# Performance work log

Hardware: AMD Instinct MI355X
Metric: run time of the kernel (lower is better)

## Reference

```python
import jax, jax.numpy as jnp
import numpy as np

B, T, C = 1024, 50, 66   # batch, frames, motion dim
H = 1024                 # LSTM state size
EPS = 1e-5               # LN_v2 epsilon


def _lstm_cell(x, h, c, W_ih, W_hh, b):
    # PyTorch gate order: input, forget, cell, output
    g = x @ W_ih.T + h @ W_hh.T + b            # [B, 4H]
    i, f, gg, o = jnp.split(g, 4, axis=-1)
    i = jax.nn.sigmoid(i)
    f = jax.nn.sigmoid(f)
    gg = jnp.tanh(gg)
    o = jax.nn.sigmoid(o)
    c2 = f * c + i * gg
    h2 = o * jnp.tanh(c2)
    return h2, c2


def setup_inputs() -> dict:
    key = jax.random.key(0)
    ks = jax.random.split(key, 12)
    s = 1.0 / np.sqrt(H)  # PyTorch LSTM init range
    return {
        "x": jax.random.normal(ks[0], (B, T, C), jnp.float32),
        # layer 0 (input_size=C); b folds PyTorch b_ih + b_hh (same math)
        "W_ih0": jax.random.uniform(ks[1], (4 * H, C), jnp.float32, -s, s),
        "W_hh0": jax.random.uniform(ks[2], (4 * H, H), jnp.float32, -s, s),
        "b0": jax.random.uniform(ks[3], (4 * H,), jnp.float32, -s, s),
        # layer 1 (input_size=H)
        "W_ih1": jax.random.uniform(ks[4], (4 * H, H), jnp.float32, -s, s),
        "W_hh1": jax.random.uniform(ks[5], (4 * H, H), jnp.float32, -s, s),
        "b1": jax.random.uniform(ks[6], (4 * H,), jnp.float32, -s, s),
        # fc0: xavier with gain 1e-8 -> near-zero weights; small scale here
        "fc_w": jax.random.normal(ks[7], (C, H), jnp.float32) * 1e-3,
        "fc_b": jnp.zeros((C,), jnp.float32),
        # LN_v2 params
        "alpha": jnp.ones((C,), jnp.float32),
        "beta": jnp.zeros((C,), jnp.float32),
    }


def reference(x, W_ih0, W_hh0, b0, W_ih1, W_hh1, b1, fc_w, fc_b, alpha, beta):
    z = jnp.zeros((x.shape[0], H), x.dtype)

    def stack(xt, h0, c0, h1, c1):
        h0, c0 = _lstm_cell(xt, h0, c0, W_ih0, W_hh0, b0)
        h1, c1 = _lstm_cell(h0, h1, c1, W_ih1, W_hh1, b1)
        return h0, c0, h1, c1

    # Encoder: consume x[:, :-1, :], keep final (h, c) of both layers
    def enc_step(carry, xt):
        return stack(xt, *carry), None

    carry, _ = jax.lax.scan(enc_step, (z, z, z, z),
                            jnp.swapaxes(x[:, :-1, :], 0, 1))

    def ln(v):  # LN_v2: layernorm over last dim, learnable alpha/beta
        m = v.mean(-1, keepdims=True)
        var = ((v - m) ** 2).mean(-1, keepdims=True)
        return (v - m) / jnp.sqrt(var + EPS) * alpha + beta

    def dec_step(carry, _):
        h0, c0, h1, c1, dec = carry
        h0, c0, h1, c1 = stack(dec, h0, c0, h1, c1)
        delta = h1 @ fc_w.T + fc_b            # fc0
        new = ln(delta) + dec                 # recursive_residual=True
        return (h0, c0, h1, c1, new), new

    dec0 = x[:, -1, :]
    _, outs = jax.lax.scan(dec_step, carry + (dec0,), None, length=x.shape[1])
    return jnp.swapaxes(outs, 0, 1)           # [B, T, C]
```

## Files before the change

### kernel.cpp

```cpp
#include <hip/hip_runtime.h>
#include <cstdint>
#include <cmath>

typedef unsigned short u16;
typedef __bf16 v8bf __attribute__((ext_vector_type(8)));
typedef float v4f __attribute__((ext_vector_type(4)));

__device__ __forceinline__ u16 f2bf(float f) {
    unsigned int u = __float_as_uint(f);
    u += 0x7fffu + ((u >> 16) & 1u);
    return (u16)(u >> 16);
}
__device__ __forceinline__ float sigmoidf_(float x) { return 1.0f / (1.0f + __expf(-x)); }
__device__ __forceinline__ float tanhf_(float x) {
    float e = __expf(2.0f * x);
    return 1.0f - 2.0f / (e + 1.0f);
}

__global__ __launch_bounds__(256)
void lstm_gemm(const u16* __restrict__ A1, int K1, int S1,
               const u16* __restrict__ A2, int S2,
               const u16* __restrict__ W, int Ktot,
               const float* __restrict__ bias,
               float* __restrict__ Cst,
               u16* __restrict__ Hout)
{
    __shared__ alignas(16) float smem[64 * 132];
    u16* At = (u16*)smem;
    u16* Bt = At + 64 * 64;

    const int tid  = threadIdx.x;
    const int wave = tid >> 6;
    const int lane = tid & 63;
    const int l16  = lane & 15;
    const int lq   = lane >> 4;
    const int wr   = wave >> 1;
    const int wc   = wave & 1;
    const int m0   = blockIdx.y * 64;
    const int n0   = blockIdx.x * 128;

    v4f acc[2][4];
#pragma unroll
    for (int i = 0; i < 2; ++i)
#pragma unroll
        for (int j = 0; j < 4; ++j) acc[i][j] = (v4f){0.f, 0.f, 0.f, 0.f};

    for (int k0 = 0; k0 < Ktot; k0 += 64) {
        const u16* Asrc; int kof, st;
        if (k0 < K1) { Asrc = A1; kof = k0;      st = S1; }
        else         { Asrc = A2; kof = k0 - K1; st = S2; }
#pragma unroll
        for (int r = 0; r < 2; ++r) {
            int c = tid + r * 256;
            int row = c >> 3;
            int kc  = (c & 7) ^ (row & 7);
            const u16* g = Asrc + (size_t)(m0 + row) * st + kof + kc * 8;
            __builtin_amdgcn_global_load_lds(
                (const __attribute__((address_space(1))) unsigned int*)g,
                (__attribute__((address_space(3))) unsigned int*)(At + c * 8),
                16, 0, 0);
        }
#pragma unroll
        for (int r = 0; r < 4; ++r) {
            int c = tid + r * 256;
            int row = c >> 3;
            int kc  = (c & 7) ^ (row & 7);
            const u16* g = W + (size_t)(n0 + row) * Ktot + k0 + kc * 8;
            __builtin_amdgcn_global_load_lds(
                (const __attribute__((address_space(1))) unsigned int*)g,
                (__attribute__((address_space(3))) unsigned int*)(Bt + c * 8),
                16, 0, 0);
        }
        asm volatile("s_waitcnt vmcnt(0)" ::: "memory");
        __syncthreads();

#pragma unroll
        for (int kk = 0; kk < 64; kk += 32) {
            const int kcb = kk >> 3;
            v8bf a[2], b[4];
#pragma unroll
            for (int mi = 0; mi < 2; ++mi) {
                int row = wr * 32 + mi * 16 + l16;
                int p = row * 8 + ((kcb + lq) ^ (row & 7));
                a[mi] = *(const v8bf*)(At + p * 8);
            }
#pragma unroll
            for (int ni = 0; ni < 4; ++ni) {
                int row = wc * 64 + ni * 16 + l16;
                int p = row * 8 + ((kcb + lq) ^ (row & 7));
                b[ni] = *(const v8bf*)(Bt + p * 8);
            }
#pragma unroll
            for (int mi = 0; mi < 2; ++mi)
#pragma unroll
                for (int ni = 0; ni < 4; ++ni)
                    acc[mi][ni] = __builtin_amdgcn_mfma_f32_16x16x32_bf16(
                        a[mi], b[ni], acc[mi][ni], 0, 0, 0);
        }
        __syncthreads();
    }

    float* gates = smem;
#pragma unroll
    for (int mi = 0; mi < 2; ++mi)
#pragma unroll
        for (int ni = 0; ni < 4; ++ni) {
            int col = wc * 64 + ni * 16 + l16;
            float bs = bias[n0 + col];
#pragma unroll
            for (int r = 0; r < 4; ++r) {
                int row = wr * 32 + mi * 16 + lq * 4 + r;
                gates[row * 132 + col] = acc[mi][ni][r] + bs;
            }
        }
    __syncthreads();

#pragma unroll
    for (int it = tid; it < 64 * 32; it += 256) {
        int row = it >> 5, u = it & 31;
        const float* gp = gates + row * 132 + u * 4;
        float gi = gp[0], gf = gp[1], gg = gp[2], go = gp[3];
        int b = m0 + row;
        int U = (n0 >> 2) + u;
        float c  = Cst[b * 1024 + U];
        float i_ = sigmoidf_(gi);
        float f_ = sigmoidf_(gf);
        float g_ = tanhf_(gg);
        float o_ = sigmoidf_(go);
        float c2 = f_ * c + i_ * g_;
        float h  = o_ * tanhf_(c2);
        Cst[b * 1024 + U]  = c2;
        Hout[b * 1024 + U] = f2bf(h);
    }
}

__global__ __launch_bounds__(256)
void fc_ln_kernel(const u16* __restrict__ H1, const u16* __restrict__ Wf,
                  const float* __restrict__ fcb, const float* __restrict__ alpha,
                  const float* __restrict__ beta,
                  const float* __restrict__ decprev, float* __restrict__ outp,
                  u16* __restrict__ decnext)
{
    const int tid  = threadIdx.x;
    const int wave = tid >> 6, lane = tid & 63;
    const int l16  = lane & 15, lq = lane >> 4;
    const int b0   = blockIdx.x * 64 + wave * 16;

    v4f acc[5];
#pragma unroll
    for (int i = 0; i < 5; ++i) acc[i] = (v4f){0.f, 0.f, 0.f, 0.f};

    for (int k = 0; k < 1024; k += 32) {
        v8bf a = *(const v8bf*)(H1 + (size_t)(b0 + l16) * 1024 + k + lq * 8);
#pragma unroll
        for (int ni = 0; ni < 5; ++ni) {
            v8bf bb = *(const v8bf*)(Wf + (size_t)(ni * 16 + l16) * 1024 + k + lq * 8);
            acc[ni] = __builtin_amdgcn_mfma_f32_16x16x32_bf16(a, bb, acc[ni], 0, 0, 0);
        }
    }

    float av[5], bv[5], fb[5]; int valid[5];
#pragma unroll
    for (int ni = 0; ni < 5; ++ni) {
        int col = ni * 16 + l16;
        valid[ni] = col < 66;
        fb[ni] = valid[ni] ? fcb[col]   : 0.f;
        av[ni] = valid[ni] ? alpha[col] : 0.f;
        bv[ni] = valid[ni] ? beta[col]  : 0.f;
    }
#pragma unroll
    for (int r = 0; r < 4; ++r) {
        int b = b0 + lq * 4 + r;
        float d[5];
        float s = 0.f;
#pragma unroll
        for (int ni = 0; ni < 5; ++ni) {
            d[ni] = valid[ni] ? (acc[ni][r] + fb[ni]) : 0.f;
            s += d[ni];
        }
#pragma unroll
        for (int m = 1; m < 16; m <<= 1) s += __shfl_xor(s, m, 64);
        float mean = s * (1.f / 66.f);
        float vs = 0.f;
#pragma unroll
        for (int ni = 0; ni < 5; ++ni) {
            float t = valid[ni] ? (d[ni] - mean) : 0.f;
            vs += t * t;
        }
#pragma unroll
        for (int m = 1; m < 16; m <<= 1) vs += __shfl_xor(vs, m, 64);
        float inv = rsqrtf(vs * (1.f / 66.f) + 1e-5f);
#pragma unroll
        for (int ni = 0; ni < 5; ++ni) {
            if (valid[ni]) {
                int col = ni * 16 + l16;
                float y = (d[ni] - mean) * inv * av[ni] + bv[ni]
                        + decprev[(size_t)b * 3300 + col];
                outp[(size_t)b * 3300 + col] = y;
                decnext[b * 128 + col] = f2bf(y);
            }
        }
    }
}

__global__ void k_init_w0(const float* __restrict__ Wih, const float* __restrict__ Whh,
                          u16* __restrict__ Wc)
{
    int idx = blockIdx.x * 256 + threadIdx.x;
    if (idx >= 4096 * 1152) return;
    int jp = idx / 1152, k = idx - jp * 1152;
    int u = jp >> 2, g = jp & 3;
    float v = 0.f;
    if (k < 66)        v = Wih[(g * 1024 + u) * 66 + k];
    else if (k >= 128) v = Whh[(size_t)(g * 1024 + u) * 1024 + (k - 128)];
    Wc[idx] = f2bf(v);
}
__global__ void k_init_w1(const float* __restrict__ Wih, const float* __restrict__ Whh,
                          u16* __restrict__ Wc)
{
    int idx = blockIdx.x * 256 + threadIdx.x;
    int jp = idx >> 11, k = idx & 2047;
    int u = jp >> 2, g = jp & 3;
    float v = (k < 1024) ? Wih[(size_t)(g * 1024 + u) * 1024 + k]
                         : Whh[(size_t)(g * 1024 + u) * 1024 + (k - 1024)];
    Wc[idx] = f2bf(v);
}
__global__ void k_init_fcw(const float* __restrict__ fcw, u16* __restrict__ Wb)
{
    int idx = blockIdx.x * 256 + threadIdx.x;
    int r = idx >> 10, k = idx & 1023;
    float v = (r < 66) ? fcw[(size_t)r * 1024 + k] : 0.f;
    Wb[idx] = f2bf(v);
}
__global__ void k_init_bias(const float* __restrict__ b0, const float* __restrict__ b1,
                            float* __restrict__ B0p, float* __restrict__ B1p)
{
    int idx = blockIdx.x * 256 + threadIdx.x;
    if (idx < 4096) B0p[idx] = b0[(idx & 3) * 1024 + (idx >> 2)];
    else { int j = idx - 4096; B1p[j] = b1[(j & 3) * 1024 + (j >> 2)]; }
}
__global__ void k_init_x(const float* __restrict__ x, u16* __restrict__ Xbuf,
                         u16* __restrict__ DEC0)
{
    int idx = blockIdx.x * 256 + threadIdx.x;
    int t = idx >> 17;
    int b = (idx >> 7) & 1023;
    int c = idx & 127;
    float v = (c < 66) ? x[(size_t)b * 3300 + t * 66 + c] : 0.f;
    u16 h = f2bf(v);
    if (t < 49) Xbuf[idx] = h;
    else        DEC0[b * 128 + c] = h;
}
__global__ void k_init_state(u16* __restrict__ H0z, u16* __restrict__ H1z,
                             float* __restrict__ C0, float* __restrict__ C1,
                             u16* __restrict__ DEC1)
{
    int idx = blockIdx.x * 256 + threadIdx.x;
    H0z[idx] = 0; H1z[idx] = 0;
    C0[idx] = 0.f; C1[idx] = 0.f;
    if (idx < 1024 * 128) DEC1[idx] = 0;
}

extern "C" void kernel_launch(void* const* d_in, const int* in_sizes, int n_in,
                              void* d_out, int out_size, void* d_ws, size_t ws_size,
                              hipStream_t stream)
{
    const float* x     = (const float*)d_in[0];
    const float* Wih0  = (const float*)d_in[1];
    const float* Whh0  = (const float*)d_in[2];
    const float* b0    = (const float*)d_in[3];
    const float* Wih1  = (const float*)d_in[4];
    const float* Whh1  = (const float*)d_in[5];
    const float* b1    = (const float*)d_in[6];
    const float* fcw   = (const float*)d_in[7];
    const float* fcb   = (const float*)d_in[8];
    const float* alpha = (const float*)d_in[9];
    const float* beta  = (const float*)d_in[10];
    float* out = (float*)d_out;

    char* p = (char*)d_ws;
    auto take = [&](size_t bytes) { char* r = p; p += (bytes + 255) & ~(size_t)255; return r; };
    u16*   Wc0  = (u16*)take((size_t)4096 * 1152 * 2);
    u16*   Wc1  = (u16*)take((size_t)4096 * 2048 * 2);
    u16*   fcwb = (u16*)take((size_t)80 * 1024 * 2);
    float* B0p  = (float*)take(4096 * 4);
    float* B1p  = (float*)take(4096 * 4);
    u16*   Xbuf = (u16*)take((size_t)49 * 1024 * 128 * 2);
    u16*   DEC  = (u16*)take((size_t)2 * 1024 * 128 * 2);
    u16*   H0   = (u16*)take((size_t)2 * 1024 * 1024 * 2);
    u16*   H1   = (u16*)take((size_t)2 * 1024 * 1024 * 2);
    float* C0   = (float*)take((size_t)1024 * 1024 * 4);
    float* C1   = (float*)take((size_t)1024 * 1024 * 4);

    k_init_w0<<<18432, 256, 0, stream>>>(Wih0, Whh0, Wc0);
    k_init_w1<<<32768, 256, 0, stream>>>(Wih1, Whh1, Wc1);
    k_init_fcw<<<320, 256, 0, stream>>>(fcw, fcwb);
    k_init_bias<<<32, 256, 0, stream>>>(b0, b1, B0p, B1p);
    k_init_x<<<25600, 256, 0, stream>>>(x, Xbuf, DEC);
    k_init_state<<<4096, 256, 0, stream>>>(H0, H1, C0, C1, DEC + 1024 * 128);

    const size_t HSZ = 1024 * 1024;
    dim3 ggrid(32, 16);
    for (int s = 0; s < 99; ++s) {
        const u16* A1;
        if (s < 49) A1 = Xbuf + (size_t)s * (1024 * 128);
        else        A1 = DEC + (size_t)((s - 49) & 1) * (1024 * 128);
        u16* h0r = H0 + (size_t)(s & 1) * HSZ;
        u16* h0w = H0 + (size_t)((s + 1) & 1) * HSZ;
        u16* h1r = H1 + (size_t)(s & 1) * HSZ;
        u16* h1w = H1 + (size_t)((s + 1) & 1) * HSZ;

        lstm_gemm<<<ggrid, 256, 0, stream>>>(A1, 128, 128, h0r, 1024,
                                             Wc0, 1152, B0p, C0, h0w);
        lstm_gemm<<<ggrid, 256, 0, stream>>>(h0w, 1024, 1024, h1r, 1024,
                                             Wc1, 2048, B1p, C1, h1w);
        if (s >= 49) {
            int d = s - 49;
            const float* decprev = (d == 0) ? (x + 49 * 66) : (out + (size_t)(d - 1) * 66);
            fc_ln_kernel<<<dim3(16), 256, 0, stream>>>(h1w, fcwb, fcb, alpha, beta,
                                                       decprev, out + (size_t)d * 66,
                                                       DEC + (size_t)((d + 1) & 1) * (1024 * 128));
        }
    }
}
```

Measured before the change: 6.751 ms.

## Enlarge LSTM GEMM tile to 128x128 and double-buffer LDS staging

The fused LSTM gate GEMM now uses 128-row M tiles instead of 64, so each block does 4x4 MFMA tiles per wave and the grid shrinks to 32x8 blocks. This halves how often each weight tile is re-read from global memory. K tiles are now prefetched into a second LDS buffer while the current one is computed, hiding load latency behind the MFMAs. Because LDS is reused for gates, the epilogue runs in two 64-row passes. Costs are 64KB of LDS per block, more accumulator registers and only 256 blocks, which reduces occupancy and latency hiding.

```diff
diff --git a/kernel.cpp b/kernel.cpp
--- a/kernel.cpp
+++ b/kernel.cpp
@@ -25,35 +25,38 @@
                float* __restrict__ Cst,
                u16* __restrict__ Hout)
 {
-    __shared__ alignas(16) float smem[64 * 132];
-    u16* At = (u16*)smem;
-    u16* Bt = At + 64 * 64;
+    __shared__ alignas(16) u16 smem[32768];
 
     const int tid  = threadIdx.x;
     const int wave = tid >> 6;
     const int lane = tid & 63;
     const int l16  = lane & 15;
     const int lq   = lane >> 4;
-    const int wr   = wave >> 1;
-    const int wc   = wave & 1;
-    const int m0   = blockIdx.y * 64;
+    const int wrb  = (wave >> 1) * 64;
+    const int wcb  = (wave & 1) * 64;
+    const int m0   = blockIdx.y * 128;
     const int n0   = blockIdx.x * 128;
 
-    v4f acc[2][4];
-#pragma unroll
-    for (int i = 0; i < 2; ++i)
+    v4f acc[4][4];
+#pragma unroll
+    for (int i = 0; i < 4; ++i)
 #pragma unroll
         for (int j = 0; j < 4; ++j) acc[i][j] = (v4f){0.f, 0.f, 0.f, 0.f};
 
-    for (int k0 = 0; k0 < Ktot; k0 += 64) {
+    const int srow = tid >> 3;
+    const int skc  = tid & 7;
+
+    auto stage_tile = [&](int k0, int buf) {
+        u16* At = smem + buf * 16384;
+        u16* Bt = At + 8192;
         const u16* Asrc; int kof, st;
         if (k0 < K1) { Asrc = A1; kof = k0;      st = S1; }
         else         { Asrc = A2; kof = k0 - K1; st = S2; }
 #pragma unroll
-        for (int r = 0; r < 2; ++r) {
+        for (int r = 0; r < 4; ++r) {
             int c = tid + r * 256;
-            int row = c >> 3;
-            int kc  = (c & 7) ^ (row & 7);
+            int row = srow + r * 32;
+            int kc  = skc ^ (row & 7);
             const u16* g = Asrc + (size_t)(m0 + row) * st + kof + kc * 8;
             __builtin_amdgcn_global_load_lds(
                 (const __attribute__((address_space(1))) unsigned int*)g,
@@ -63,74 +66,86 @@
 #pragma unroll
         for (int r = 0; r < 4; ++r) {
             int c = tid + r * 256;
-            int row = c >> 3;
-            int kc  = (c & 7) ^ (row & 7);
+            int row = srow + r * 32;
+            int kc  = skc ^ (row & 7);
             const u16* g = W + (size_t)(n0 + row) * Ktot + k0 + kc * 8;
             __builtin_amdgcn_global_load_lds(
                 (const __attribute__((address_space(1))) unsigned int*)g,
                 (__attribute__((address_space(3))) unsigned int*)(Bt + c * 8),
                 16, 0, 0);
         }
-        asm volatile("s_waitcnt vmcnt(0)" ::: "memory");
+    };
+
+    const int nt = Ktot >> 6;
+    stage_tile(0, 0);
+    for (int it = 0; it < nt; ++it) {
         __syncthreads();
-
+        if (it + 1 < nt) stage_tile((it + 1) << 6, (it + 1) & 1);
+        const u16* At = smem + (it & 1) * 16384;
+        const u16* Bt = At + 8192;
 #pragma unroll
         for (int kk = 0; kk < 64; kk += 32) {
             const int kcb = kk >> 3;
-            v8bf a[2], b[4];
-#pragma unroll
-            for (int mi = 0; mi < 2; ++mi) {
-                int row = wr * 32 + mi * 16 + l16;
+            v8bf a[4], b[4];
+#pragma unroll
+            for (int mi = 0; mi < 4; ++mi) {
+                int row = wrb + mi * 16 + l16;
                 int p = row * 8 + ((kcb + lq) ^ (row & 7));
                 a[mi] = *(const v8bf*)(At + p * 8);
             }
 #pragma unroll
             for (int ni = 0; ni < 4; ++ni) {
-                int row = wc * 64 + ni * 16 + l16;
+                int row = wcb + ni * 16 + l16;
                 int p = row * 8 + ((kcb + lq) ^ (row & 7));
                 b[ni] = *(const v8bf*)(Bt + p * 8);
             }
 #pragma unroll
-            for (int mi = 0; mi < 2; ++mi)
+            for (int mi = 0; mi < 4; ++mi)
 #pragma unroll
                 for (int ni = 0; ni < 4; ++ni)
                     acc[mi][ni] = __builtin_amdgcn_mfma_f32_16x16x32_bf16(
                         a[mi], b[ni], acc[mi][ni], 0, 0, 0);
         }
+    }
+    __syncthreads();
+
+    float* gates = (float*)smem;
+#pragma unroll
+    for (int p = 0; p < 2; ++p) {
+        if ((wave >> 1) == p) {
+#pragma unroll
+            for (int mi = 0; mi < 4; ++mi)
+#pragma unroll
+                for (int ni = 0; ni < 4; ++ni) {
+                    int col = wcb + ni * 16 + l16;
+                    float bs = bias[n0 + col];
+#pragma unroll
+                    for (int r = 0; r < 4; ++r) {
+                        int row = mi * 16 + lq * 4 + r;
+                        gates[row * 132 + col] = acc[mi][ni][r] + bs;
+                    }
+                }
+        }
         __syncthreads();
-    }
-
-    float* gates = smem;
-#pragma unroll
-    for (int mi = 0; mi < 2; ++mi)
-#pragma unroll
-        for (int ni = 0; ni < 4; ++ni) {
-            int col = wc * 64 + ni * 16 + l16;
-            float bs = bias[n0 + col];
-#pragma unroll
-            for (int r = 0; r < 4; ++r) {
-                int row = wr * 32 + mi * 16 + lq * 4 + r;
-                gates[row * 132 + col] = acc[mi][ni][r] + bs;
-            }
-        }
-    __syncthreads();
-
-#pragma unroll
-    for (int it = tid; it < 64 * 32; it += 256) {
-        int row = it >> 5, u = it & 31;
-        const float* gp = gates + row * 132 + u * 4;
-        float gi = gp[0], gf = gp[1], gg = gp[2], go = gp[3];
-        int b = m0 + row;
-        int U = (n0 >> 2) + u;
-        float c  = Cst[b * 1024 + U];
-        float i_ = sigmoidf_(gi);
-        float f_ = sigmoidf_(gf);
-        float g_ = tanhf_(gg);
-        float o_ = sigmoidf_(go);
-        float c2 = f_ * c + i_ * g_;
-        float h  = o_ * tanhf_(c2);
-        Cst[b * 1024 + U]  = c2;
-        Hout[b * 1024 + U] = f2bf(h);
+#pragma unroll
+        for (int j = 0; j < 8; ++j) {
+            int it2 = tid + j * 256;
+            int row = it2 >> 5, u = it2 & 31;
+            const float* gp = gates + row * 132 + u * 4;
+            float gi = gp[0], gf = gp[1], gg = gp[2], go = gp[3];
+            int b = m0 + p * 64 + row;
+            int U = (n0 >> 2) + u;
+            float c  = Cst[b * 1024 + U];
+            float i_ = sigmoidf_(gi);
+            float f_ = sigmoidf_(gf);
+            float g_ = tanhf_(gg);
+            float o_ = sigmoidf_(go);
+            float c2 = f_ * c + i_ * g_;
+            float h  = o_ * tanhf_(c2);
+            Cst[b * 1024 + U]  = c2;
+            Hout[b * 1024 + U] = f2bf(h);
+        }
+        __syncthreads();
     }
 }
 
@@ -300,7 +315,7 @@
     k_init_state<<<4096, 256, 0, stream>>>(H0, H1, C0, C1, DEC + 1024 * 128);
 
     const size_t HSZ = 1024 * 1024;
-    dim3 ggrid(32, 16);
+    dim3 ggrid(32, 8);
     for (int s = 0; s < 99; ++s) {
         const u16* A1;
         if (s < 49) A1 = Xbuf + (size_t)s * (1024 * 128);
```

Measured after the change: 6.607 ms. 2.1% less time.
